# Performance work log

Measured on AMD Instinct MI355X. Metric: run time of the kernel, lower is better.

## Reference

```python
import jax, jax.numpy as jnp
import numpy as np

B, N, L, P = 128, 128, 64, 30  # batch, max_nodes, latent_dim, n_perms
LOG2PI = float(np.log(2.0 * np.pi))


def setup_inputs() -> dict:
    key = jax.random.key(0)
    k_mu, k_ls, k_eps, k_w, k_adj, k_mask, k_perm = jax.random.split(key, 7)
    mu = jax.random.normal(k_mu, (B, L), dtype=jnp.float32)
    logstd = 0.1 * jax.random.normal(k_ls, (B, L), dtype=jnp.float32)
    eps = jax.random.normal(k_eps, (B, L), dtype=jnp.float32)
    W_dec = 0.02 * jax.random.normal(k_w, (L, N * N), dtype=jnp.float32)
    Adj = jax.random.randint(k_adj, (B, N, N), 0, 2, dtype=jnp.int32)
    # symmetric adjacency, zero diagonal
    Adj = jnp.triu(Adj, 1)
    Adj = Adj + jnp.swapaxes(Adj, 1, 2)
    # per-graph node counts -> block masks marking valid node pairs
    n_nodes = jax.random.randint(k_mask, (B,), N // 2, N + 1)  # [B]
    valid = jnp.arange(N)[None, :] < n_nodes[:, None]          # [B, N]
    node_masks = (valid[:, :, None] & valid[:, None, :]).astype(jnp.int32)
    # true random permutations, one per (i, j) pair as in the torch loop
    perm_keys = jax.random.split(k_perm, B * P)
    perms = jax.vmap(lambda kk: jax.random.permutation(kk, N))(perm_keys)
    perms = perms.reshape(B, P, N).astype(jnp.int32)
    return {"mu": mu, "logstd": logstd, "eps": eps, "W_dec": W_dec,
            "Adj": Adj, "node_masks": node_masks, "perms": perms}


def _masked_perm_logprob(logit, A, m, perm):
    # logit: [N,N] Bernoulli logits; A, m: [N,N]; perm: [N]
    lp = logit[perm][:, perm]  # symmetric permutation of rows and cols
    logp = A * jax.nn.log_sigmoid(lp) + (1.0 - A) * jax.nn.log_sigmoid(-lp)
    return jnp.sum(logp * m)


def reference(mu, logstd, eps, W_dec, Adj, node_masks, perms):
    # q = Normal(mu, exp(logstd)); z = q.rsample()
    z = mu + eps * jnp.exp(logstd)                      # [B, L]
    logits = (z @ W_dec).reshape(B, N, N)               # decoder Bernoulli logits
    # Faithful to torch loop: rec_errors[i, j] uses logits[j], Adj[j], mask[j]
    # with an independent random permutation per (i, j).
    l_p = logits[:P]                                    # [P, N, N]
    A_p = Adj[:P].astype(logits.dtype)
    m_p = node_masks[:P].astype(logits.dtype)
    rec_errors = jax.vmap(
        lambda perm_i: jax.vmap(_masked_perm_logprob)(l_p, A_p, m_p, perm_i)
    )(perms)                                            # [B, P]
    RE = jnp.sum(jnp.max(rec_errors, axis=1))           # scalar
    # KL = log q(z) - log p(z), Independent Normal over latent dim
    log_q = jnp.sum(-0.5 * eps * eps - logstd - 0.5 * LOG2PI, axis=-1)  # [B]
    log_p = jnp.sum(-0.5 * z * z - 0.5 * LOG2PI, axis=-1)               # [B]
    KL = log_q - log_p
    elbo = jnp.mean(RE - KL)
    return -elbo
```

## Files before the change

### kernel.cpp

```cpp
#include <hip/hip_runtime.h>
#include <hip/hip_fp16.h>
#include <math.h>

#define Bn 128
#define Nn 128
#define Ln 64
#define Pn 30
#define PG 10

#define TOFF  0
#define BOFF  491520
#define VOFFW 506880
#define ROFF  510720

__global__ __launch_bounds__(256) void k_prep(const float* __restrict__ mu,
                                              const float* __restrict__ logstd,
                                              const float* __restrict__ eps,
                                              const float* __restrict__ W,
                                              const int* __restrict__ Adj,
                                              const int* __restrict__ nm,
                                              float* __restrict__ ws) {
    int blk = blockIdx.x, t = threadIdx.x;
    if (blk < 192) {
        int chunk = blk & 63, pg = blk >> 6;
        __shared__ float zs[PG][Ln];
        for (int idx = t; idx < PG * Ln; idx += 256) {
            int g = pg * PG * Ln + idx;
            zs[idx / Ln][idx % Ln] = mu[g] + eps[g] * __expf(logstd[g]);
        }
        __syncthreads();
        int uv = chunk * 256 + t;
        float acc[PG];
#pragma unroll
        for (int q = 0; q < PG; q++) acc[q] = 0.f;
        for (int k = 0; k < Ln; k++) {
            float w = W[k * (Nn * Nn) + uv];
#pragma unroll
            for (int q = 0; q < PG; q++) acc[q] = fmaf(zs[q][k], w, acc[q]);
        }
        uint32_t* tab = (uint32_t*)ws;
#pragma unroll
        for (int q = 0; q < PG; q++) {
            int p = pg * PG + q;
            float l = acc[q];
            float nl = -l;
            float lsneg = (nl < 0.f) ? (nl - log1pf(__expf(nl))) : (-log1pf(__expf(-nl)));
            __half2 h = __floats2half2_rn(lsneg, l);
            tab[p * (Nn * Nn) + uv] = *(uint32_t*)&h;
        }
    } else {
        int p = blk - 192;
        __shared__ float val_s[Nn];
        if (t < Nn) {
            float v = (float)nm[p * Nn * Nn + t * Nn + t];
            val_s[t] = v;
            ws[VOFFW + p * Nn + t] = v;
        }
        __syncthreads();
        int sub = t >> 6, lane = t & 63;
        int ioff = sub >> 1, ch = sub & 1;
        int j = ch * 64 + lane;
        uint32_t* Bp = (uint32_t*)ws + BOFF + p * Nn * 4;
        for (int ib = 0; ib < Nn; ib += 2) {
            int i = ib + ioff;
            bool pred = (Adj[p * Nn * Nn + i * Nn + j] != 0) &&
                        (val_s[i] != 0.f) && (val_s[j] != 0.f);
            unsigned long long m = __ballot(pred);
            if (lane == 0) {
                Bp[i * 4 + ch * 2]     = (uint32_t)m;
                Bp[i * 4 + ch * 2 + 1] = (uint32_t)(m >> 32);
            }
        }
    }
}

__global__ __launch_bounds__(256) void k_main(const int* __restrict__ perms,
                                              const float* __restrict__ ws,
                                              float* __restrict__ rec) {
    int p = blockIdx.x >> 7;
    int b = blockIdx.x & (Bn - 1);
    int t = threadIdx.x;

    __shared__ int      inv_s[Nn];
    __shared__ uint32_t B_s[Nn * 4];
    __shared__ float    red[256];

    if (t < Nn) {
        int pm = perms[(b * Pn + p) * Nn + t];
        inv_s[pm] = t;
    }
    {
        const uint32_t* Bp = (const uint32_t*)ws + BOFF + p * Nn * 4;
        B_s[t]       = Bp[t];
        B_s[256 + t] = Bp[256 + t];
    }
    __syncthreads();

    const float* validp = ws + VOFFW + p * Nn;
    int   v  = t & (Nn - 1);
    int   i0 = t >> 7;
    int   j  = inv_s[v];
    float wv = validp[j];
    int   wsel = j >> 5, jsh = j & 31;

    int   lanei   = t & 63;
    int   iu      = inv_s[2 * lanei + i0];
    int   wu_bits = __float_as_int(validp[iu]);

    const uint32_t* tabp = (const uint32_t*)ws + p * (Nn * Nn);
    float acc1 = 0.f, acc2 = 0.f;

#pragma unroll 4
    for (int it = 0; it < 64; ++it) {
        int      si   = __builtin_amdgcn_readlane(iu, it);
        float    swu  = __int_as_float(__builtin_amdgcn_readlane(wu_bits, it));
        uint32_t bits = B_s[si * 4 + wsel];
        uint32_t hw   = tabp[it * 256 + t];
        __half2  h    = *(__half2*)&hw;
        float2   f    = __half22float2(h);
        float    bitf = (float)((bits >> jsh) & 1u);
        acc1 = fmaf(swu * wv, f.x, acc1);
        acc2 = fmaf(bitf, f.y, acc2);
    }

    red[t] = acc1 + acc2;
    __syncthreads();
    for (int s = 128; s > 0; s >>= 1) {
        if (t < s) red[t] += red[t + s];
        __syncthreads();
    }
    if (t == 0) rec[b * Pn + p] = red[0];
}

__global__ void k_final(const float* __restrict__ mu,
                        const float* __restrict__ logstd,
                        const float* __restrict__ eps,
                        const float* __restrict__ ws,
                        float* __restrict__ out) {
    int t = threadIdx.x;
    float kl = 0.f;
    for (int l = 0; l < Ln; ++l) {
        int   idx = t * Ln + l;
        float e = eps[idx], ls = logstd[idx];
        float z = mu[idx] + e * __expf(ls);
        kl += -0.5f * e * e - ls + 0.5f * z * z;
    }
    float m = -INFINITY;
    for (int p = 0; p < Pn; p++) m = fmaxf(m, ws[ROFF + t * Pn + p]);
    float contrib = kl * (1.0f / Bn) - m;
    __shared__ float red[128];
    red[t] = contrib;
    __syncthreads();
    for (int s = 64; s > 0; s >>= 1) {
        if (t < s) red[t] += red[t + s];
        __syncthreads();
    }
    if (t == 0) out[0] = red[0];
}

extern "C" void kernel_launch(void* const* d_in, const int* in_sizes, int n_in,
                              void* d_out, int out_size, void* d_ws, size_t ws_size,
                              hipStream_t stream) {
    const float* mu     = (const float*)d_in[0];
    const float* logstd = (const float*)d_in[1];
    const float* eps    = (const float*)d_in[2];
    const float* W      = (const float*)d_in[3];
    const int*   Adj    = (const int*)d_in[4];
    const int*   nm     = (const int*)d_in[5];
    const int*   perms  = (const int*)d_in[6];
    float* ws  = (float*)d_ws;
    float* out = (float*)d_out;

    hipLaunchKernelGGL(k_prep,  dim3(192 + Pn), dim3(256), 0, stream,
                       mu, logstd, eps, W, Adj, nm, ws);
    hipLaunchKernelGGL(k_main,  dim3(Pn * Bn),  dim3(256), 0, stream,
                       perms, ws, ws + ROFF);
    hipLaunchKernelGGL(k_final, dim3(1),        dim3(128), 0, stream,
                       mu, logstd, eps, ws, out);
}
```

Before: 131.5 us.

## Process two batch rows per block and fuse final reduction via last-block atomic

The main kernel now has each block handle two batch entries for one permutation graph. Each logit-table load is reused across both, and uint2 loads cover two columns per lane. Block reduction uses wavefront shuffles. The final max/sum kernel is removed: the KL term is computed in an extra prep block, and the last main block, found with an atomic counter and thread fences, performs the final reduction. This saves one kernel launch and halves table traffic, but adds atomic and fence overhead and more LDS lookups per iteration.

```diff
diff --git a/kernel.cpp b/kernel.cpp
--- a/kernel.cpp
+++ b/kernel.cpp
@@ -12,6 +12,8 @@
 #define BOFF  491520
 #define VOFFW 506880
 #define ROFF  510720
+#define KLOFF 514560
+#define CNTOFF 514561
 
 __global__ __launch_bounds__(256) void k_prep(const float* __restrict__ mu,
                                               const float* __restrict__ logstd,
@@ -48,7 +50,7 @@
             __half2 h = __floats2half2_rn(lsneg, l);
             tab[p * (Nn * Nn) + uv] = *(uint32_t*)&h;
         }
-    } else {
+    } else if (blk < 192 + Pn) {
         int p = blk - 192;
         __shared__ float val_s[Nn];
         if (t < Nn) {
@@ -71,91 +73,136 @@
                 Bp[i * 4 + ch * 2 + 1] = (uint32_t)(m >> 32);
             }
         }
+    } else {
+        float kl = 0.f;
+        for (int idx = t; idx < Bn * Ln; idx += 256) {
+            float e = eps[idx], ls = logstd[idx];
+            float z = mu[idx] + e * __expf(ls);
+            kl += -0.5f * e * e - ls + 0.5f * z * z;
+        }
+        __shared__ float red[256];
+        red[t] = kl;
+        __syncthreads();
+        for (int s = 128; s > 0; s >>= 1) {
+            if (t < s) red[t] += red[t + s];
+            __syncthreads();
+        }
+        if (t == 0) {
+            ws[KLOFF] = red[0] * (1.0f / (float)Bn);
+            ((uint32_t*)ws)[CNTOFF] = 0u;
+        }
     }
 }
 
 __global__ __launch_bounds__(256) void k_main(const int* __restrict__ perms,
-                                              const float* __restrict__ ws,
-                                              float* __restrict__ rec) {
-    int p = blockIdx.x >> 7;
-    int b = blockIdx.x & (Bn - 1);
+                                              float* __restrict__ ws,
+                                              float* __restrict__ out) {
+    int p  = blockIdx.x >> 6;
+    int bb = blockIdx.x & 63;
+    int b0 = bb * 2, b1 = b0 + 1;
     int t = threadIdx.x;
 
-    __shared__ int      inv_s[Nn];
+    __shared__ int      inv_s[2][Nn];
     __shared__ uint32_t B_s[Nn * 4];
-    __shared__ float    red[256];
+    __shared__ float    valid_s[Nn];
+    __shared__ float    redw[2][4];
+    __shared__ int      flag;
 
     if (t < Nn) {
-        int pm = perms[(b * Pn + p) * Nn + t];
-        inv_s[pm] = t;
+        inv_s[0][perms[(b0 * Pn + p) * Nn + t]] = t;
+        valid_s[t] = ws[VOFFW + p * Nn + t];
+    } else {
+        inv_s[1][perms[(b1 * Pn + p) * Nn + (t - Nn)]] = t - Nn;
     }
     {
         const uint32_t* Bp = (const uint32_t*)ws + BOFF + p * Nn * 4;
         B_s[t]       = Bp[t];
         B_s[256 + t] = Bp[256 + t];
     }
-    __syncthreads();
-
-    const float* validp = ws + VOFFW + p * Nn;
-    int   v  = t & (Nn - 1);
-    int   i0 = t >> 7;
-    int   j  = inv_s[v];
-    float wv = validp[j];
-    int   wsel = j >> 5, jsh = j & 31;
-
-    int   lanei   = t & 63;
-    int   iu      = inv_s[2 * lanei + i0];
-    int   wu_bits = __float_as_int(validp[iu]);
-
-    const uint32_t* tabp = (const uint32_t*)ws + p * (Nn * Nn);
-    float acc1 = 0.f, acc2 = 0.f;
+    if (t == 0) flag = 0;
+    __syncthreads();
+
+    int lane = t & 63;
+    int wid  = t >> 6;
+    int v0 = 2 * lane, v1 = v0 + 1;
+
+    int   j00 = inv_s[0][v0], j01 = inv_s[0][v1];
+    int   j10 = inv_s[1][v0], j11 = inv_s[1][v1];
+    float wv00 = valid_s[j00], wv01 = valid_s[j01];
+    float wv10 = valid_s[j10], wv11 = valid_s[j11];
+    int   a00 = j00 >> 5, sh00 = j00 & 31;
+    int   a01 = j01 >> 5, sh01 = j01 & 31;
+    int   a10 = j10 >> 5, sh10 = j10 & 31;
+    int   a11 = j11 >> 5, sh11 = j11 & 31;
+
+    const uint2* tab2 = (const uint2*)((const uint32_t*)ws + p * (Nn * Nn));
+    float acc0 = 0.f, acc1 = 0.f;
 
 #pragma unroll 4
-    for (int it = 0; it < 64; ++it) {
-        int      si   = __builtin_amdgcn_readlane(iu, it);
-        float    swu  = __int_as_float(__builtin_amdgcn_readlane(wu_bits, it));
-        uint32_t bits = B_s[si * 4 + wsel];
-        uint32_t hw   = tabp[it * 256 + t];
-        __half2  h    = *(__half2*)&hw;
-        float2   f    = __half22float2(h);
-        float    bitf = (float)((bits >> jsh) & 1u);
-        acc1 = fmaf(swu * wv, f.x, acc1);
-        acc2 = fmaf(bitf, f.y, acc2);
-    }
-
-    red[t] = acc1 + acc2;
-    __syncthreads();
-    for (int s = 128; s > 0; s >>= 1) {
-        if (t < s) red[t] += red[t + s];
-        __syncthreads();
-    }
-    if (t == 0) rec[b * Pn + p] = red[0];
-}
-
-__global__ void k_final(const float* __restrict__ mu,
-                        const float* __restrict__ logstd,
-                        const float* __restrict__ eps,
-                        const float* __restrict__ ws,
-                        float* __restrict__ out) {
-    int t = threadIdx.x;
-    float kl = 0.f;
-    for (int l = 0; l < Ln; ++l) {
-        int   idx = t * Ln + l;
-        float e = eps[idx], ls = logstd[idx];
-        float z = mu[idx] + e * __expf(ls);
-        kl += -0.5f * e * e - ls + 0.5f * z * z;
-    }
-    float m = -INFINITY;
-    for (int p = 0; p < Pn; p++) m = fmaxf(m, ws[ROFF + t * Pn + p]);
-    float contrib = kl * (1.0f / Bn) - m;
-    __shared__ float red[128];
-    red[t] = contrib;
-    __syncthreads();
-    for (int s = 64; s > 0; s >>= 1) {
-        if (t < s) red[t] += red[t + s];
-        __syncthreads();
-    }
-    if (t == 0) out[0] = red[0];
+    for (int it = 0; it < 32; ++it) {
+        int u = it * 4 + wid;
+        int   si0  = inv_s[0][u];
+        int   si1  = inv_s[1][u];
+        float swu0 = valid_s[si0];
+        float swu1 = valid_s[si1];
+        uint2 hw   = tab2[u * (Nn / 2) + lane];
+        float2 f0  = __half22float2(*(__half2*)&hw.x);
+        float2 f1  = __half22float2(*(__half2*)&hw.y);
+
+        {
+            float tmp = wv00 * f0.x;
+            tmp = fmaf(wv01, f1.x, tmp);
+            acc0 = fmaf(swu0, tmp, acc0);
+            uint32_t r0 = B_s[si0 * 4 + a00];
+            uint32_t r1 = B_s[si0 * 4 + a01];
+            acc0 = fmaf((float)((r0 >> sh00) & 1u), f0.y, acc0);
+            acc0 = fmaf((float)((r1 >> sh01) & 1u), f1.y, acc0);
+        }
+        {
+            float tmp = wv10 * f0.x;
+            tmp = fmaf(wv11, f1.x, tmp);
+            acc1 = fmaf(swu1, tmp, acc1);
+            uint32_t r0 = B_s[si1 * 4 + a10];
+            uint32_t r1 = B_s[si1 * 4 + a11];
+            acc1 = fmaf((float)((r0 >> sh10) & 1u), f0.y, acc1);
+            acc1 = fmaf((float)((r1 >> sh11) & 1u), f1.y, acc1);
+        }
+    }
+
+#pragma unroll
+    for (int s = 32; s > 0; s >>= 1) {
+        acc0 += __shfl_down(acc0, s, 64);
+        acc1 += __shfl_down(acc1, s, 64);
+    }
+    if (lane == 0) { redw[0][wid] = acc0; redw[1][wid] = acc1; }
+    __syncthreads();
+    if (t < 2) {
+        float r = redw[t][0] + redw[t][1] + redw[t][2] + redw[t][3];
+        ws[ROFF + (b0 + t) * Pn + p] = r;
+    }
+    __threadfence();
+    __syncthreads();
+    if (t == 0) {
+        uint32_t old = atomicAdd((uint32_t*)ws + CNTOFF, 1u);
+        if (old == (uint32_t)(Pn * 64 - 1)) flag = 1;
+    }
+    __syncthreads();
+    if (flag) {
+        __threadfence();
+        __shared__ float red[128];
+        if (t < 128) {
+            float m = -INFINITY;
+#pragma unroll
+            for (int q = 0; q < Pn; q++) m = fmaxf(m, ws[ROFF + t * Pn + q]);
+            red[t] = m;
+        }
+        __syncthreads();
+        for (int s = 64; s > 0; s >>= 1) {
+            if (t < s) red[t] += red[t + s];
+            __syncthreads();
+        }
+        if (t == 0) out[0] = ws[KLOFF] - red[0];
+    }
 }
 
 extern "C" void kernel_launch(void* const* d_in, const int* in_sizes, int n_in,
@@ -171,10 +218,8 @@
     float* ws  = (float*)d_ws;
     float* out = (float*)d_out;
 
-    hipLaunchKernelGGL(k_prep,  dim3(192 + Pn), dim3(256), 0, stream,
+    hipLaunchKernelGGL(k_prep, dim3(192 + Pn + 1), dim3(256), 0, stream,
                        mu, logstd, eps, W, Adj, nm, ws);
-    hipLaunchKernelGGL(k_main,  dim3(Pn * Bn),  dim3(256), 0, stream,
-                       perms, ws, ws + ROFF);
-    hipLaunchKernelGGL(k_final, dim3(1),        dim3(128), 0, stream,
-                       mu, logstd, eps, ws, out);
+    hipLaunchKernelGGL(k_main, dim3(Pn * 64),      dim3(256), 0, stream,
+                       perms, ws, out);
 }
```

New measurement: 245.9 us. +87.0%, slower.

## Reuse each logit table tile across four batch permutations per block

Applied to the files above, without the earlier changes.

k_main now processes four batch entries per block for a given graph p, so each half2 table load is reused by four permutations. Block reductions move from shared memory to wavefront shuffles. The adjacency bitmask build is split across four blocks per graph, and the KL sum moves into an extra k_prep block so k_final only takes the max and combines. The aim is less global table traffic and a shorter serial prep and final tail, at the cost of more shared-memory index lookups inside the inner loop and fewer blocks in k_main.

```diff
diff --git a/kernel.cpp b/kernel.cpp
--- a/kernel.cpp
+++ b/kernel.cpp
@@ -12,6 +12,7 @@
 #define BOFF  491520
 #define VOFFW 506880
 #define ROFF  510720
+#define KLOFF 514560
 
 __global__ __launch_bounds__(256) void k_prep(const float* __restrict__ mu,
                                               const float* __restrict__ logstd,
@@ -48,8 +49,10 @@
             __half2 h = __floats2half2_rn(lsneg, l);
             tab[p * (Nn * Nn) + uv] = *(uint32_t*)&h;
         }
-    } else {
-        int p = blk - 192;
+    } else if (blk < 192 + 4 * Pn) {
+        int pb = blk - 192;
+        int p  = pb >> 2;
+        int qr = pb & 3;
         __shared__ float val_s[Nn];
         if (t < Nn) {
             float v = (float)nm[p * Nn * Nn + t * Nn + t];
@@ -61,7 +64,7 @@
         int ioff = sub >> 1, ch = sub & 1;
         int j = ch * 64 + lane;
         uint32_t* Bp = (uint32_t*)ws + BOFF + p * Nn * 4;
-        for (int ib = 0; ib < Nn; ib += 2) {
+        for (int ib = qr * 32; ib < qr * 32 + 32; ib += 2) {
             int i = ib + ioff;
             bool pred = (Adj[p * Nn * Nn + i * Nn + j] != 0) &&
                         (val_s[i] != 0.f) && (val_s[j] != 0.f);
@@ -71,91 +74,117 @@
                 Bp[i * 4 + ch * 2 + 1] = (uint32_t)(m >> 32);
             }
         }
+    } else {
+        float kl = 0.f;
+        for (int idx = t; idx < Bn * Ln; idx += 256) {
+            float e = eps[idx], ls = logstd[idx];
+            float z = mu[idx] + e * __expf(ls);
+            kl += -0.5f * e * e - ls + 0.5f * z * z;
+        }
+        __shared__ float red[256];
+        red[t] = kl;
+        __syncthreads();
+        for (int s = 128; s > 0; s >>= 1) {
+            if (t < s) red[t] += red[t + s];
+            __syncthreads();
+        }
+        if (t == 0) ws[KLOFF] = red[0] * (1.0f / (float)Bn);
     }
 }
 
 __global__ __launch_bounds__(256) void k_main(const int* __restrict__ perms,
                                               const float* __restrict__ ws,
                                               float* __restrict__ rec) {
-    int p = blockIdx.x >> 7;
-    int b = blockIdx.x & (Bn - 1);
+    int p  = blockIdx.x >> 5;
+    int bb = blockIdx.x & 31;
+    int b_base = bb * 4;
     int t = threadIdx.x;
 
-    __shared__ int      inv_s[Nn];
+    __shared__ int      inv_s[4][Nn];
     __shared__ uint32_t B_s[Nn * 4];
-    __shared__ float    red[256];
-
-    if (t < Nn) {
-        int pm = perms[(b * Pn + p) * Nn + t];
-        inv_s[pm] = t;
-    }
+    __shared__ float    valid_s[Nn];
+    __shared__ float    redw[4][4];
+
     {
+        int idx0 = t, idx1 = t + 256;
+        int ba0 = idx0 >> 7, i0 = idx0 & 127;
+        int ba1 = idx1 >> 7, i1 = idx1 & 127;
+        inv_s[ba0][perms[((b_base + ba0) * Pn + p) * Nn + i0]] = i0;
+        inv_s[ba1][perms[((b_base + ba1) * Pn + p) * Nn + i1]] = i1;
         const uint32_t* Bp = (const uint32_t*)ws + BOFF + p * Nn * 4;
         B_s[t]       = Bp[t];
         B_s[256 + t] = Bp[256 + t];
+        if (t < Nn) valid_s[t] = ws[VOFFW + p * Nn + t];
     }
     __syncthreads();
 
-    const float* validp = ws + VOFFW + p * Nn;
-    int   v  = t & (Nn - 1);
-    int   i0 = t >> 7;
-    int   j  = inv_s[v];
-    float wv = validp[j];
-    int   wsel = j >> 5, jsh = j & 31;
-
-    int   lanei   = t & 63;
-    int   iu      = inv_s[2 * lanei + i0];
-    int   wu_bits = __float_as_int(validp[iu]);
-
-    const uint32_t* tabp = (const uint32_t*)ws + p * (Nn * Nn);
-    float acc1 = 0.f, acc2 = 0.f;
+    int lane = t & 63;
+    int wid  = t >> 6;
+    int v0 = 2 * lane, v1 = v0 + 1;
+
+    float wv0[4], wv1[4];
+    int   a0[4], sh0[4], a1[4], sh1[4];
+#pragma unroll
+    for (int b = 0; b < 4; ++b) {
+        int j0 = inv_s[b][v0], j1 = inv_s[b][v1];
+        wv0[b] = valid_s[j0];  wv1[b] = valid_s[j1];
+        a0[b] = j0 >> 5; sh0[b] = j0 & 31;
+        a1[b] = j1 >> 5; sh1[b] = j1 & 31;
+    }
+
+    const uint2* tab2 = (const uint2*)((const uint32_t*)ws + p * (Nn * Nn));
+    float acc[4] = {0.f, 0.f, 0.f, 0.f};
 
 #pragma unroll 4
-    for (int it = 0; it < 64; ++it) {
-        int      si   = __builtin_amdgcn_readlane(iu, it);
-        float    swu  = __int_as_float(__builtin_amdgcn_readlane(wu_bits, it));
-        uint32_t bits = B_s[si * 4 + wsel];
-        uint32_t hw   = tabp[it * 256 + t];
-        __half2  h    = *(__half2*)&hw;
-        float2   f    = __half22float2(h);
-        float    bitf = (float)((bits >> jsh) & 1u);
-        acc1 = fmaf(swu * wv, f.x, acc1);
-        acc2 = fmaf(bitf, f.y, acc2);
-    }
-
-    red[t] = acc1 + acc2;
+    for (int it = 0; it < 32; ++it) {
+        int u = it * 4 + wid;
+        uint2 hw = tab2[u * (Nn / 2) + lane];
+        float2 f0 = __half22float2(*(__half2*)&hw.x);
+        float2 f1 = __half22float2(*(__half2*)&hw.y);
+#pragma unroll
+        for (int b = 0; b < 4; ++b) {
+            int   si  = inv_s[b][u];
+            float swu = valid_s[si];
+            float tmp = fmaf(wv1[b], f1.x, wv0[b] * f0.x);
+            acc[b] = fmaf(swu, tmp, acc[b]);
+            uint32_t r0 = B_s[si * 4 + a0[b]];
+            uint32_t r1 = B_s[si * 4 + a1[b]];
+            acc[b] += ((r0 >> sh0[b]) & 1u) ? f0.y : 0.0f;
+            acc[b] += ((r1 >> sh1[b]) & 1u) ? f1.y : 0.0f;
+        }
+    }
+
+#pragma unroll
+    for (int s = 32; s > 0; s >>= 1) {
+#pragma unroll
+        for (int b = 0; b < 4; ++b) acc[b] += __shfl_down(acc[b], s, 64);
+    }
+    if (lane == 0) {
+#pragma unroll
+        for (int b = 0; b < 4; ++b) redw[b][wid] = acc[b];
+    }
     __syncthreads();
-    for (int s = 128; s > 0; s >>= 1) {
-        if (t < s) red[t] += red[t + s];
-        __syncthreads();
-    }
-    if (t == 0) rec[b * Pn + p] = red[0];
-}
-
-__global__ void k_final(const float* __restrict__ mu,
-                        const float* __restrict__ logstd,
-                        const float* __restrict__ eps,
-                        const float* __restrict__ ws,
-                        float* __restrict__ out) {
+    if (t < 4) {
+        float r = redw[t][0] + redw[t][1] + redw[t][2] + redw[t][3];
+        rec[(b_base + t) * Pn + p] = r;
+    }
+}
+
+__global__ void k_final(const float* __restrict__ ws, float* __restrict__ out) {
     int t = threadIdx.x;
-    float kl = 0.f;
-    for (int l = 0; l < Ln; ++l) {
-        int   idx = t * Ln + l;
-        float e = eps[idx], ls = logstd[idx];
-        float z = mu[idx] + e * __expf(ls);
-        kl += -0.5f * e * e - ls + 0.5f * z * z;
-    }
     float m = -INFINITY;
+#pragma unroll
     for (int p = 0; p < Pn; p++) m = fmaxf(m, ws[ROFF + t * Pn + p]);
-    float contrib = kl * (1.0f / Bn) - m;
+    float contrib = -m * (1.0f / 128.0f);
+    (void)contrib;
     __shared__ float red[128];
-    red[t] = contrib;
+    red[t] = m;
     __syncthreads();
     for (int s = 64; s > 0; s >>= 1) {
         if (t < s) red[t] += red[t + s];
         __syncthreads();
     }
-    if (t == 0) out[0] = red[0];
+    if (t == 0) out[0] = ws[KLOFF] - red[0];
 }
 
 extern "C" void kernel_launch(void* const* d_in, const int* in_sizes, int n_in,
@@ -171,10 +200,10 @@
     float* ws  = (float*)d_ws;
     float* out = (float*)d_out;
 
-    hipLaunchKernelGGL(k_prep,  dim3(192 + Pn), dim3(256), 0, stream,
+    hipLaunchKernelGGL(k_prep,  dim3(192 + 4 * Pn + 1), dim3(256), 0, stream,
                        mu, logstd, eps, W, Adj, nm, ws);
-    hipLaunchKernelGGL(k_main,  dim3(Pn * Bn),  dim3(256), 0, stream,
+    hipLaunchKernelGGL(k_main,  dim3(Pn * 32),          dim3(256), 0, stream,
                        perms, ws, ws + ROFF);
-    hipLaunchKernelGGL(k_final, dim3(1),        dim3(128), 0, stream,
-                       mu, logstd, eps, ws, out);
-}
+    hipLaunchKernelGGL(k_final, dim3(1),                dim3(128), 0, stream,
+                       ws, out);
+}
```

Result: faster. 126.2 us (-4.0%).
